# Kernel optimization log

Hardware: AMD Instinct MI355X
Metric: run time of the kernel (lower is better)

The kernel has to match this reference:

```python
import jax, jax.numpy as jnp
import numpy as np

NUM_CLASSES = 80
STRIDES = (8, 16, 32)
FEATS = ((80, 80), (40, 40), (20, 20))
RADIUS = 2.5
CAND_K = 10


def make_grids():
    grids, strides = [], []
    for (h, w), s in zip(FEATS, STRIDES):
        gx, gy = jnp.meshgrid(jnp.arange(w), jnp.arange(h))  # xy indexing: gx=col, gy=row
        g = jnp.stack([gx, gy], -1).reshape(-1, 2).astype(jnp.float32)
        grids.append(g)
        strides.append(jnp.full((h * w, 1), float(s), jnp.float32))
    return jnp.concatenate(grids, 0), jnp.concatenate(strides, 0)  # [A,2], [A,1]


def decode_level(p, s):
    # p: [B, 85, h, w] -> decoded [B, h*w, 85]; xy/wh decoded, conf/cls stay logits
    b, c, h, w = p.shape
    out = p.reshape(b, c, h * w).transpose(0, 2, 1)
    gx, gy = jnp.meshgrid(jnp.arange(w), jnp.arange(h))
    g = jnp.stack([gx, gy], -1).reshape(1, -1, 2).astype(p.dtype)
    xy = (out[..., :2] + g) * s
    wh = jnp.exp(out[..., 2:4]) * s
    return jnp.concatenate([xy, wh, out[..., 4:]], -1)


def pairwise_iou_cxcywh(a, b):
    # a: [G,4], b: [A,4] -> [G,A]
    tl = jnp.maximum(a[:, None, :2] - a[:, None, 2:] * 0.5, b[None, :, :2] - b[None, :, 2:] * 0.5)
    br = jnp.minimum(a[:, None, :2] + a[:, None, 2:] * 0.5, b[None, :, :2] + b[None, :, 2:] * 0.5)
    wh = jnp.clip(br - tl, 0.0)
    inter = wh[..., 0] * wh[..., 1]
    area_a = (a[:, 2] * a[:, 3])[:, None]
    area_b = (b[:, 2] * b[:, 3])[None, :]
    return inter / (area_a + area_b - inter + 1e-16)


def elem_iou_cxcywh(a, b):
    # a, b: [...,4] aligned -> [...]
    tl = jnp.maximum(a[..., :2] - a[..., 2:] * 0.5, b[..., :2] - b[..., 2:] * 0.5)
    br = jnp.minimum(a[..., :2] + a[..., 2:] * 0.5, b[..., :2] + b[..., 2:] * 0.5)
    wh = jnp.clip(br - tl, 0.0)
    inter = wh[..., 0] * wh[..., 1]
    area = a[..., 2] * a[..., 3] + b[..., 2] * b[..., 3]
    return inter / (area - inter + 1e-16)


def bce_logits(x, t):
    return jnp.maximum(x, 0.0) - x * t + jnp.log1p(jnp.exp(-jnp.abs(x)))


def assign_one(gt_b, gt_c, pbox, pconf, pcls, xy_center, stride_v):
    # SimOTA dynamic matching for one image. gt_b:[G,4], gt_c:[G], pbox:[A,4], pconf:[A,1], pcls:[A,C]
    G = gt_b.shape[0]
    # center-in-box / center-in-mirror(radius) masks
    bmin = gt_b[:, :2] - gt_b[:, 2:] * 0.5
    bmax = gt_b[:, :2] + gt_b[:, 2:] * 0.5
    d = jnp.concatenate([xy_center[None] - bmin[:, None], bmax[:, None] - xy_center[None]], -1)  # [G,A,4]
    in_box = jnp.min(d, -1) > 0.0
    mmin = gt_b[:, None, :2] - RADIUS * stride_v[None]
    mmax = gt_b[:, None, :2] + RADIUS * stride_v[None]
    d2 = jnp.concatenate([xy_center[None] - mmin, mmax - xy_center[None]], -1)
    in_mir = jnp.min(d2, -1) > 0.0
    union = jnp.any(in_box, 0) | jnp.any(in_mir, 0)  # [A]
    inter = in_box & in_mir  # [G,A]

    iou = pairwise_iou_cxcywh(gt_b, pbox)  # [G,A]
    iou_cost = -jnp.log(iou + 1e-8)
    # cls cost: BCE(sqrt(sigmoid(cls)*sigmoid(conf)), one_hot).sum(C), computed without [G,A,C]
    p = jnp.sqrt(jax.nn.sigmoid(pcls) * jax.nn.sigmoid(pconf))  # [A,C]
    logp = jnp.clip(jnp.log(jnp.clip(p, 1e-12)), -100.0)
    log1mp = jnp.clip(jnp.log(jnp.clip(1.0 - p, 1e-12)), -100.0)
    cls_cost = -(logp[:, gt_c].T - log1mp[:, gt_c].T + log1mp.sum(-1)[None, :])  # [G,A]

    cost = cls_cost + 3.0 * iou_cost + 1e5 * (~inter).astype(cost_dtype(pcls))
    cost = jnp.where(union[None, :], cost, 1e15)  # exclude anchors outside union (bool-index in torch)
    iou_m = jnp.where(union[None, :], iou, 0.0)

    # dynamic k per gt = clamp(int(sum top10 iou), 1)
    topk_iou, _ = jax.lax.top_k(iou_m, CAND_K)
    dyn_k = jnp.maximum(topk_iou.sum(1).astype(jnp.int32), 1)  # [G]
    _, idx = jax.lax.top_k(-cost, CAND_K)  # smallest-cost anchors per gt [G,10]
    valid = (jnp.arange(CAND_K)[None, :] < dyn_k[:, None]).astype(cost.dtype)
    mm = jnp.zeros_like(cost).at[jnp.arange(G)[:, None], idx].set(valid)  # [G,A]

    # resolve anchors matched to >1 gt by argmin cost
    multi = mm.sum(0) > 1.0
    best = jnp.argmin(cost, 0)  # [A]
    mm = jnp.where(multi[None, :], jax.nn.one_hot(best, G, dtype=mm.dtype).T, mm)

    fg = mm.sum(0) > 0.0  # [A]
    gt_idx = jnp.argmax(mm, 0)  # [A]
    match_iou = (mm * iou).sum(0)  # [A]
    return fg, gt_idx, match_iou


def cost_dtype(x):
    return x.dtype


def setup_inputs() -> dict:
    key = jax.random.key(0)
    ks = jax.random.split(key, 5)
    B, G = 32, 16
    p8 = jax.random.normal(ks[0], (B, 85, 80, 80), jnp.float32)
    p16 = jax.random.normal(ks[1], (B, 85, 40, 40), jnp.float32)
    p32 = jax.random.normal(ks[2], (B, 85, 20, 20), jnp.float32)
    u = jax.random.uniform(ks[3], (B, G, 4), jnp.float32)
    gt_boxes = jnp.concatenate([32.0 + u[..., :2] * 576.0, 16.0 + u[..., 2:] * 112.0], -1)
    gt_cls = jax.random.randint(ks[4], (B, G), 0, 80, dtype=jnp.int32)
    return {"p8": p8, "p16": p16, "p32": p32, "gt_boxes": gt_boxes, "gt_cls": gt_cls}


def reference(p8, p16, p32, gt_boxes, gt_cls):
    outs = [decode_level(p, s) for p, s in zip((p8, p16, p32), STRIDES)]
    outputs = jnp.concatenate(outs, 1)  # [B, 8400, 85]
    grids, stride_v = make_grids()
    xy_center = (grids + 0.5) * stride_v  # [A,2]
    pbox, pconf, pcls = outputs[..., :4], outputs[..., 4:5], outputs[..., 5:]

    sg = jax.lax.stop_gradient  # assignment is under torch.no_grad
    fg, gt_idx, match_iou = jax.vmap(assign_one, in_axes=(0, 0, 0, 0, 0, None, None))(
        gt_boxes, gt_cls, sg(pbox), sg(pconf), sg(pcls), xy_center, stride_v)
    match_iou = sg(match_iou)

    tgt_box = jnp.take_along_axis(gt_boxes, gt_idx[..., None], axis=1)  # [B,A,4]
    tgt_cls_id = jnp.take_along_axis(gt_cls, gt_idx, axis=1)  # [B,A]
    tgt_cls = jax.nn.one_hot(tgt_cls_id, NUM_CLASSES, dtype=outputs.dtype) * match_iou[..., None]
    fgf = fg.astype(outputs.dtype)

    iou_e = elem_iou_cxcywh(pbox, tgt_box)  # [B,A]
    loss_box = jnp.sum(fgf * (1.0 - iou_e ** 2))            # IOUloss, fg only
    loss_conf = jnp.sum(bce_logits(pconf[..., 0], fgf))     # all anchors
    loss_cls = jnp.sum(fgf[..., None] * bce_logits(pcls, tgt_cls))  # fg only
    n_fg = jnp.maximum(jnp.sum(fgf), 1.0)
    return (5.0 * loss_box + loss_conf + loss_cls) / n_fg
```

## Files before the change

kernel.cpp:

```cpp
#include <hip/hip_runtime.h>
#include <hip/hip_bf16.h>

#define A_TOT 8400
#define NB 32
#define NG 16
#define NC 80

#define K1_GX 33
#define NWAVE (K1_GX * NB * 4)
#define K3_CH 8
#define K3_W  1050

#define L2E 1.44269504088896340736f
#define LN2 0.69314718055994530942f

__device__ inline float fexp2(float x) { return __builtin_amdgcn_exp2f(x); }
__device__ inline float flog2(float x) { return __builtin_amdgcn_logf(x); }
__device__ inline float frcp(float x)  { return __builtin_amdgcn_rcpf(x); }
__device__ inline float fsqrtf_(float x) { return __builtin_amdgcn_sqrtf(x); }

__device__ inline float iou_cxcywh(float acx, float acy, float aw, float ah,
                                   float bcx, float bcy, float bw, float bh) {
    float tlx = fmaxf(acx - aw * 0.5f, bcx - bw * 0.5f);
    float tly = fmaxf(acy - ah * 0.5f, bcy - bh * 0.5f);
    float brx = fminf(acx + aw * 0.5f, bcx + bw * 0.5f);
    float bry = fminf(acy + ah * 0.5f, bcy + bh * 0.5f);
    float w = fmaxf(brx - tlx, 0.0f);
    float h = fmaxf(bry - tly, 0.0f);
    float inter = w * h;
    return inter / (aw * ah + bw * bh - inter + 1e-16f);
}

__device__ inline float dval_of(float x, float sc) {
    float u = fexp2(-x * L2E);
    float sx = frcp(1.0f + u);
    float pr = fsqrtf_(sx * sc);
    float lp  = fmaxf(LN2 * flog2(fmaxf(pr, 1e-12f)), -100.0f);
    float l1p = fmaxf(LN2 * flog2(fmaxf(1.0f - pr, 1e-12f)), -100.0f);
    return lp - l1p;
}

__device__ inline float cost_fast(float iou, float d, float sp, unsigned m, int g) {
    if (!((m >> 16) & 1u)) return 1e15f;
    float c = -(d + sp) - 3.0f * LN2 * flog2(iou + 1e-8f);
    if (!((m >> g) & 1u)) c += 100000.0f;
    return c;
}

__device__ inline unsigned long long umax64(unsigned long long a, unsigned long long b) {
    return a > b ? a : b;
}
__device__ inline unsigned long long umin64(unsigned long long a, unsigned long long b) {
    return a < b ? a : b;
}

__device__ inline const float* lvl_base(int a, int b, const float* p8, const float* p16,
                                        const float* p32, int& hw, int& HW, int& W, float& s) {
    if (a < 6400) { hw = a;        HW = 6400; W = 80; s = 8.0f;  return p8  + (size_t)b * 85 * 6400; }
    if (a < 8000) { hw = a - 6400; HW = 1600; W = 40; s = 16.0f; return p16 + (size_t)b * 85 * 1600; }
    { hw = a - 8000; HW = 400; W = 20; s = 32.0f; return p32 + (size_t)b * 85 * 400; }
}

__global__ __launch_bounds__(256) void k1_decode(
    const float* __restrict__ p8, const float* __restrict__ p16, const float* __restrict__ p32,
    const float* __restrict__ gtb,
    float4* __restrict__ pbox, float4* __restrict__ rec, float* __restrict__ part) {
    int b = blockIdx.y;
    int tid = threadIdx.x;
    int a = blockIdx.x * 256 + tid;
    float bce0_conf = 0.0f;
    if (a < A_TOT) {
        int hw, HW, W;
        float s;
        const float* base = lvl_base(a, b, p8, p16, p32, hw, HW, W, s);

        float tx = base[hw], ty = base[HW + hw];
        float tw = base[2 * HW + hw], th = base[3 * HW + hw];
        float cf = base[4 * HW + hw];
        int gx = hw % W, gy = hw / W;
        float pcx = (tx + (float)gx) * s;
        float pcy = (ty + (float)gy) * s;
        float pw = fexp2(tw * L2E) * s;
        float ph = fexp2(th * L2E) * s;

        float uc = fexp2(-cf * L2E);
        float suc = 1.0f + uc;
        float sc = frcp(suc);
        bce0_conf = cf + LN2 * flog2(suc);

        float xc = ((float)gx + 0.5f) * s;
        float yc = ((float)gy + 0.5f) * s;
        unsigned m = 0;
        bool uni = false;
        float r = 2.5f * s;
#pragma unroll 4
        for (int g = 0; g < NG; g++) {
            float gcx = gtb[(b * NG + g) * 4 + 0];
            float gcy = gtb[(b * NG + g) * 4 + 1];
            float gw  = gtb[(b * NG + g) * 4 + 2];
            float gh  = gtb[(b * NG + g) * 4 + 3];
            bool ib = (xc > gcx - gw * 0.5f) && (gcx + gw * 0.5f > xc) &&
                      (yc > gcy - gh * 0.5f) && (gcy + gh * 0.5f > yc);
            bool im = (xc > gcx - r) && (gcx + r > xc) &&
                      (yc > gcy - r) && (gcy + r > yc);
            uni |= (ib || im);
            if (ib && im) m |= (1u << g);
        }
        if (uni) m |= (1u << 16);

        float suml1p = 0.0f;
        if (uni) {
            const float* cbase = base + 5 * HW + hw;
#pragma unroll
            for (int cc = 0; cc < NC; cc += 20) {
                float x[20];
#pragma unroll
                for (int j = 0; j < 20; j++) x[j] = cbase[(cc + j) * HW];
#pragma unroll
                for (int j = 0; j < 20; j++) {
                    float u = fexp2(-x[j] * L2E);
                    float pr = fsqrtf_(frcp(1.0f + u) * sc);
                    suml1p += fmaxf(LN2 * flog2(fmaxf(1.0f - pr, 1e-12f)), -100.0f);
                }
            }
        }

        size_t i = (size_t)b * A_TOT + a;
        pbox[i] = make_float4(pcx, pcy, pw, ph);
        rec[i] = make_float4(__uint_as_float(m), sc, suml1p, cf);
    }
    float v = bce0_conf;
    for (int off = 32; off; off >>= 1) v += __shfl_down(v, off, 64);
    if ((tid & 63) == 0) {
        int wave = (blockIdx.y * gridDim.x + blockIdx.x) * 4 + (tid >> 6);
        part[wave] = v;
    }
}

__global__ __launch_bounds__(512, 4) void k2_assign(
    const float* __restrict__ gtb, const int* __restrict__ gtc,
    const float4* __restrict__ pbox, const float4* __restrict__ rec,
    const float* __restrict__ p8, const float* __restrict__ p16, const float* __restrict__ p32,
    int* __restrict__ sel, int* __restrict__ nsel) {
    __shared__ unsigned long long wred[8];
    int blk = blockIdx.x;
    int b = blk >> 4, g = blk & 15;
    int tid = threadIdx.x;

    float gcx = gtb[blk * 4 + 0], gcy = gtb[blk * 4 + 1];
    float gw = gtb[blk * 4 + 2],  gh = gtb[blk * 4 + 3];
    int cg = gtc[blk];

    unsigned long long topI[10];
    unsigned long long topC[10];
#pragma unroll
    for (int i = 0; i < 10; i++) { topI[i] = 0ull; topC[i] = 0xFFFFFFFFFFFFFFFFull; }

    for (int a = tid; a < A_TOT; a += 512) {
        size_t i = (size_t)b * A_TOT + a;
        float4 pb = pbox[i];
        float4 rc = rec[i];
        unsigned m = __float_as_uint(rc.x);
        float iou = iou_cxcywh(gcx, gcy, gw, gh, pb.x, pb.y, pb.z, pb.w);

        float cost = 1e15f;
        float mi = 0.0f;
        if ((m >> 16) & 1u) {
            mi = iou;
            int hw, HW, W;
            float s;
            const float* base = lvl_base(a, b, p8, p16, p32, hw, HW, W, s);
            float x = base[(5 + cg) * HW + hw];
            float d = dval_of(x, rc.y);
            cost = -(d + rc.z) - 3.0f * LN2 * flog2(iou + 1e-8f);
            if (!((m >> g) & 1u)) cost += 100000.0f;
        }

        if (mi > 0.0f) {
            unsigned long long kI = ((unsigned long long)__float_as_uint(mi) << 32) | (unsigned)a;
            if (kI > topI[9]) {
                unsigned long long v = kI;
#pragma unroll
                for (int i2 = 0; i2 < 10; i2++) {
                    unsigned long long big = umax64(topI[i2], v);
                    v = umin64(topI[i2], v);
                    topI[i2] = big;
                }
            }
        }
        unsigned long long kC = ((unsigned long long)__float_as_uint(cost) << 32) | (unsigned)a;
        if (kC < topC[9]) {
            unsigned long long v = kC;
#pragma unroll
            for (int i2 = 0; i2 < 10; i2++) {
                unsigned long long sml = umin64(topC[i2], v);
                v = umax64(topC[i2], v);
                topC[i2] = sml;
            }
        }
    }

    float ksum = 0.0f;
    for (int rr = 0; rr < 10; rr++) {
        unsigned long long h = topI[0];
        for (int off = 32; off; off >>= 1) h = umax64(h, __shfl_xor(h, off, 64));
        if ((tid & 63) == 0) wred[tid >> 6] = h;
        __syncthreads();
        unsigned long long w = wred[0];
#pragma unroll
        for (int j = 1; j < 8; j++) w = umax64(w, wred[j]);
        ksum += __uint_as_float((unsigned)(w >> 32));
        if (topI[0] == w) {
#pragma unroll
            for (int i = 0; i < 9; i++) topI[i] = topI[i + 1];
            topI[9] = 0ull;
        }
        __syncthreads();
    }
    int dynk = (int)ksum;
    if (dynk < 1) dynk = 1;
    if (dynk > 10) dynk = 10;

    for (int rr = 0; rr < 10; rr++) {
        unsigned long long h = topC[0];
        for (int off = 32; off; off >>= 1) h = umin64(h, __shfl_xor(h, off, 64));
        if ((tid & 63) == 0) wred[tid >> 6] = h;
        __syncthreads();
        unsigned long long w = wred[0];
#pragma unroll
        for (int j = 1; j < 8; j++) w = umin64(w, wred[j]);
        if (tid == 0) sel[blk * 10 + rr] = (int)(w & 0xffffffffu);
        if (topC[0] == w) {
#pragma unroll
            for (int i = 0; i < 9; i++) topC[i] = topC[i + 1];
            topC[9] = 0xFFFFFFFFFFFFFFFFull;
        }
        __syncthreads();
    }
    if (tid == 0) nsel[blk] = dynk;
}

__global__ __launch_bounds__(256) void k3_resolve(
    const float* __restrict__ gtb, const int* __restrict__ gtc,
    const float4* __restrict__ pbox, const float4* __restrict__ rec,
    const int* __restrict__ sel, const int* __restrict__ nsel,
    const float* __restrict__ p8, const float* __restrict__ p16, const float* __restrict__ p32,
    float4* __restrict__ part3) {
    __shared__ unsigned tag[K3_W];
    __shared__ float gb[NG * 4];
    __shared__ int gc[NG];
    __shared__ float red[256];
    int b = blockIdx.y, chunk = blockIdx.x, tid = threadIdx.x;
    int a0 = chunk * K3_W;

    for (int j = tid; j < K3_W; j += 256) tag[j] = 0;
    if (tid < NG * 4) gb[tid] = gtb[b * NG * 4 + tid];
    if (tid < NG) gc[tid] = gtc[b * NG + tid];
    __syncthreads();

    if (tid < NG * 10) {
        int g = tid / 10, k = tid % 10;
        if (k < nsel[b * NG + g]) {
            int a = sel[(b * NG + g) * 10 + k];
            if (a >= a0 && a < a0 + K3_W)
                atomicAdd(&tag[a - a0], 0x10000u + (unsigned)(g + 1));
        }
    }
    __syncthreads();

    float lbox = 0.0f, lconfc = 0.0f, lcls = 0.0f, nfg = 0.0f;
    for (int j = tid; j < K3_W; j += 256) {
        unsigned t = tag[j];
        unsigned cnt = t >> 16;
        if (!cnt) continue;
        int a = a0 + j;
        size_t i = (size_t)b * A_TOT + a;
        float4 pb = pbox[i];
        float4 rc = rec[i];
        int hw, HW, W;
        float s;
        const float* base = lvl_base(a, b, p8, p16, p32, hw, HW, W, s);
        int gs;
        if (cnt == 1) {
            gs = (int)(t & 0xffffu) - 1;
        } else {
            unsigned m = __float_as_uint(rc.x);
            float bc = 3.402823466e38f;
            gs = 0;
            for (int g = 0; g < NG; g++) {
                float iou = iou_cxcywh(gb[g * 4], gb[g * 4 + 1], gb[g * 4 + 2], gb[g * 4 + 3],
                                       pb.x, pb.y, pb.z, pb.w);
                float x = base[(5 + gc[g]) * HW + hw];
                float d = dval_of(x, rc.y);
                float c = cost_fast(iou, d, rc.z, m, g);
                if (c < bc) { bc = c; gs = g; }
            }
        }
        float miou = iou_cxcywh(gb[gs * 4], gb[gs * 4 + 1], gb[gs * 4 + 2], gb[gs * 4 + 3],
                                pb.x, pb.y, pb.z, pb.w);
        int cid = gc[gs];
        float xcid = base[(5 + cid) * HW + hw];

        float s0 = 0.0f;
        const float* cbase = base + 5 * HW + hw;
#pragma unroll
        for (int cc = 0; cc < NC; cc += 20) {
            float x[20];
#pragma unroll
            for (int jj = 0; jj < 20; jj++) x[jj] = cbase[(cc + jj) * HW];
#pragma unroll
            for (int jj = 0; jj < 20; jj++) {
                float u = fexp2(-x[jj] * L2E);
                s0 += x[jj] + LN2 * flog2(1.0f + u);
            }
        }

        lbox += 1.0f - miou * miou;
        lconfc -= rc.w;
        lcls += s0 - xcid * miou;
        nfg += 1.0f;
    }

    float vals[4] = {lbox, lconfc, lcls, nfg};
    float outv[4];
    for (int i = 0; i < 4; i++) {
        red[tid] = vals[i];
        __syncthreads();
        for (int s2 = 128; s2 > 0; s2 >>= 1) {
            if (tid < s2) red[tid] += red[tid + s2];
            __syncthreads();
        }
        outv[i] = red[0];
        __syncthreads();
    }
    if (tid == 0)
        part3[blockIdx.y * K3_CH + chunk] = make_float4(outv[0], outv[1], outv[2], outv[3]);
}

__global__ __launch_bounds__(256) void k4_final(
    const float* __restrict__ part, const float4* __restrict__ part3, float* __restrict__ out) {
    __shared__ float red[256];
    int tid = threadIdx.x;
    float v = 0.0f;
    for (int i = tid; i < NWAVE; i += 256) v += part[i];
    float4 p = part3[tid & 255];
    float vals[5] = {v, p.x, p.y, p.z, p.w};
    float tot[5];
    for (int i = 0; i < 5; i++) {
        red[tid] = vals[i];
        __syncthreads();
        for (int s2 = 128; s2 > 0; s2 >>= 1) {
            if (tid < s2) red[tid] += red[tid + s2];
            __syncthreads();
        }
        tot[i] = red[0];
        __syncthreads();
    }
    if (tid == 0) {
        float nfg = tot[4];
        if (nfg < 1.0f) nfg = 1.0f;
        out[0] = (5.0f * tot[1] + (tot[0] + tot[2]) + tot[3]) / nfg;
    }
}

extern "C" void kernel_launch(void* const* d_in, const int* in_sizes, int n_in,
                              void* d_out, int out_size, void* d_ws, size_t ws_size,
                              hipStream_t stream) {
    const float* p8  = (const float*)d_in[0];
    const float* p16 = (const float*)d_in[1];
    const float* p32 = (const float*)d_in[2];
    const float* gtb = (const float*)d_in[3];
    const int*   gtc = (const int*)d_in[4];

    char* w = (char*)d_ws;
    float4* pbox = (float4*)w;                 w += (size_t)NB * A_TOT * sizeof(float4);
    float4* rec  = (float4*)w;                 w += (size_t)NB * A_TOT * sizeof(float4);
    int* sel     = (int*)w;                    w += (size_t)NB * NG * 10 * sizeof(int);
    int* nsel    = (int*)w;                    w += (size_t)NB * NG * sizeof(int);
    float* part  = (float*)w;                  w += (size_t)NWAVE * sizeof(float);
    float4* part3 = (float4*)w;                w += (size_t)NB * K3_CH * sizeof(float4);

    k1_decode<<<dim3(K1_GX, NB), 256, 0, stream>>>(
        p8, p16, p32, gtb, pbox, rec, part);
    k2_assign<<<NB * NG, 512, 0, stream>>>(gtb, gtc, pbox, rec,
                                           p8, p16, p32, sel, nsel);
    k3_resolve<<<dim3(K3_CH, NB), 256, 0, stream>>>(gtb, gtc, pbox, rec,
                                                    sel, nsel, p8, p16, p32, part3);
    k4_final<<<1, 256, 0, stream>>>(part, part3, (float*)d_out);
}
```

Measured before the change: 185.8 us.

## Compact candidate anchors in decode, iterate only candidates in assign, fuse final reduce

The decode kernel now builds a per-image compacted list of candidate anchors (inside any GT box or radius) with shared and global atomics. It also spreads each candidate's 80-class log-sum work across four threads, so per-thread class work is balanced instead of divergent. The assign kernel iterates only that compacted list with 256 threads instead of scanning all 8400 anchors, dropping non-candidate loads and cost evaluations. The final reduction kernel is folded into the resolve kernel via a last-block-done counter, at the cost of an extra memset and atomics.

```diff
diff --git a/kernel.cpp b/kernel.cpp
--- a/kernel.cpp
+++ b/kernel.cpp
@@ -10,6 +10,7 @@
 #define NWAVE (K1_GX * NB * 4)
 #define K3_CH 8
 #define K3_W  1050
+#define K3_BLOCKS (K3_CH * NB)
 
 #define L2E 1.44269504088896340736f
 #define LN2 0.69314718055994530942f
@@ -61,15 +62,24 @@
     { hw = a - 8000; HW = 400; W = 20; s = 32.0f; return p32 + (size_t)b * 85 * 400; }
 }
 
-__global__ __launch_bounds__(256) void k1_decode(
+__global__ __launch_bounds__(256, 4) void k1_decode(
     const float* __restrict__ p8, const float* __restrict__ p16, const float* __restrict__ p32,
     const float* __restrict__ gtb,
-    float4* __restrict__ pbox, float4* __restrict__ rec, float* __restrict__ part) {
+    float4* __restrict__ pbox, float4* __restrict__ rec,
+    int* __restrict__ cmp, int* __restrict__ cnt, float* __restrict__ part) {
+    __shared__ int lcnt, base_s;
+    __shared__ int list[256];
+    __shared__ float scl[256];
     int b = blockIdx.y;
     int tid = threadIdx.x;
     int a = blockIdx.x * 256 + tid;
+    bool valid = a < A_TOT;
+    if (tid == 0) lcnt = 0;
+    __syncthreads();
+
     float bce0_conf = 0.0f;
-    if (a < A_TOT) {
+    int myslot = -1;
+    if (valid) {
         int hw, HW, W;
         float s;
         const float* base = lvl_base(a, b, p8, p16, p32, hw, HW, W, s);
@@ -106,29 +116,49 @@
             uni |= (ib || im);
             if (ib && im) m |= (1u << g);
         }
-        if (uni) m |= (1u << 16);
-
-        float suml1p = 0.0f;
         if (uni) {
-            const float* cbase = base + 5 * HW + hw;
-#pragma unroll
-            for (int cc = 0; cc < NC; cc += 20) {
-                float x[20];
-#pragma unroll
-                for (int j = 0; j < 20; j++) x[j] = cbase[(cc + j) * HW];
-#pragma unroll
-                for (int j = 0; j < 20; j++) {
-                    float u = fexp2(-x[j] * L2E);
-                    float pr = fsqrtf_(frcp(1.0f + u) * sc);
-                    suml1p += fmaxf(LN2 * flog2(fmaxf(1.0f - pr, 1e-12f)), -100.0f);
-                }
-            }
-        }
-
+            m |= (1u << 16);
+            myslot = atomicAdd(&lcnt, 1);
+            list[myslot] = tid;
+            scl[myslot] = sc;
+        }
         size_t i = (size_t)b * A_TOT + a;
         pbox[i] = make_float4(pcx, pcy, pw, ph);
-        rec[i] = make_float4(__uint_as_float(m), sc, suml1p, cf);
-    }
+        rec[i] = make_float4(__uint_as_float(m), sc, 0.0f, cf);
+    }
+    __syncthreads();
+    int n = lcnt;
+    if (tid == 0) base_s = atomicAdd(&cnt[b], n);
+    __syncthreads();
+    if (myslot >= 0) cmp[(size_t)b * A_TOT + base_s + myslot] = a;
+
+    for (int t = tid; t < n * 4; t += 256) {
+        int slot = t >> 2, q = t & 3;
+        int lt = list[slot];
+        int aa = blockIdx.x * 256 + lt;
+        float sc2 = scl[slot];
+        int hw, HW, W;
+        float s;
+        const float* base = lvl_base(aa, b, p8, p16, p32, hw, HW, W, s);
+        const float* cbase = base + (5 + q * 20) * HW + hw;
+        float x[20];
+#pragma unroll
+        for (int j = 0; j < 20; j++) x[j] = cbase[j * HW];
+        float suml1p = 0.0f;
+#pragma unroll
+        for (int j = 0; j < 20; j++) {
+            float u = fexp2(-x[j] * L2E);
+            float pr = fsqrtf_(frcp(1.0f + u) * sc2);
+            suml1p += fmaxf(LN2 * flog2(fmaxf(1.0f - pr, 1e-12f)), -100.0f);
+        }
+        suml1p += __shfl_xor(suml1p, 1, 64);
+        suml1p += __shfl_xor(suml1p, 2, 64);
+        if (q == 0) {
+            float* recf = (float*)rec;
+            recf[((size_t)b * A_TOT + aa) * 4 + 2] = suml1p;
+        }
+    }
+
     float v = bce0_conf;
     for (int off = 32; off; off >>= 1) v += __shfl_down(v, off, 64);
     if ((tid & 63) == 0) {
@@ -137,12 +167,13 @@
     }
 }
 
-__global__ __launch_bounds__(512, 4) void k2_assign(
+__global__ __launch_bounds__(256, 4) void k2_assign(
     const float* __restrict__ gtb, const int* __restrict__ gtc,
     const float4* __restrict__ pbox, const float4* __restrict__ rec,
+    const int* __restrict__ cmp, const int* __restrict__ cnt,
     const float* __restrict__ p8, const float* __restrict__ p16, const float* __restrict__ p32,
     int* __restrict__ sel, int* __restrict__ nsel) {
-    __shared__ unsigned long long wred[8];
+    __shared__ unsigned long long wred[4];
     int blk = blockIdx.x;
     int b = blk >> 4, g = blk & 15;
     int tid = threadIdx.x;
@@ -150,34 +181,31 @@
     float gcx = gtb[blk * 4 + 0], gcy = gtb[blk * 4 + 1];
     float gw = gtb[blk * 4 + 2],  gh = gtb[blk * 4 + 3];
     int cg = gtc[blk];
+    int n = cnt[b];
 
     unsigned long long topI[10];
     unsigned long long topC[10];
 #pragma unroll
     for (int i = 0; i < 10; i++) { topI[i] = 0ull; topC[i] = 0xFFFFFFFFFFFFFFFFull; }
 
-    for (int a = tid; a < A_TOT; a += 512) {
+    for (int j = tid; j < n; j += 256) {
+        int a = cmp[(size_t)b * A_TOT + j];
         size_t i = (size_t)b * A_TOT + a;
         float4 pb = pbox[i];
         float4 rc = rec[i];
         unsigned m = __float_as_uint(rc.x);
         float iou = iou_cxcywh(gcx, gcy, gw, gh, pb.x, pb.y, pb.z, pb.w);
 
-        float cost = 1e15f;
-        float mi = 0.0f;
-        if ((m >> 16) & 1u) {
-            mi = iou;
-            int hw, HW, W;
-            float s;
-            const float* base = lvl_base(a, b, p8, p16, p32, hw, HW, W, s);
-            float x = base[(5 + cg) * HW + hw];
-            float d = dval_of(x, rc.y);
-            cost = -(d + rc.z) - 3.0f * LN2 * flog2(iou + 1e-8f);
-            if (!((m >> g) & 1u)) cost += 100000.0f;
-        }
-
-        if (mi > 0.0f) {
-            unsigned long long kI = ((unsigned long long)__float_as_uint(mi) << 32) | (unsigned)a;
+        int hw, HW, W;
+        float s;
+        const float* base = lvl_base(a, b, p8, p16, p32, hw, HW, W, s);
+        float x = base[(5 + cg) * HW + hw];
+        float d = dval_of(x, rc.y);
+        float cost = -(d + rc.z) - 3.0f * LN2 * flog2(iou + 1e-8f);
+        if (!((m >> g) & 1u)) cost += 100000.0f;
+
+        if (iou > 0.0f) {
+            unsigned long long kI = ((unsigned long long)__float_as_uint(iou) << 32) | (unsigned)a;
             if (kI > topI[9]) {
                 unsigned long long v = kI;
 #pragma unroll
@@ -206,9 +234,7 @@
         for (int off = 32; off; off >>= 1) h = umax64(h, __shfl_xor(h, off, 64));
         if ((tid & 63) == 0) wred[tid >> 6] = h;
         __syncthreads();
-        unsigned long long w = wred[0];
-#pragma unroll
-        for (int j = 1; j < 8; j++) w = umax64(w, wred[j]);
+        unsigned long long w = umax64(umax64(wred[0], wred[1]), umax64(wred[2], wred[3]));
         ksum += __uint_as_float((unsigned)(w >> 32));
         if (topI[0] == w) {
 #pragma unroll
@@ -226,9 +252,7 @@
         for (int off = 32; off; off >>= 1) h = umin64(h, __shfl_xor(h, off, 64));
         if ((tid & 63) == 0) wred[tid >> 6] = h;
         __syncthreads();
-        unsigned long long w = wred[0];
-#pragma unroll
-        for (int j = 1; j < 8; j++) w = umin64(w, wred[j]);
+        unsigned long long w = umin64(umin64(wred[0], wred[1]), umin64(wred[2], wred[3]));
         if (tid == 0) sel[blk * 10 + rr] = (int)(w & 0xffffffffu);
         if (topC[0] == w) {
 #pragma unroll
@@ -245,11 +269,13 @@
     const float4* __restrict__ pbox, const float4* __restrict__ rec,
     const int* __restrict__ sel, const int* __restrict__ nsel,
     const float* __restrict__ p8, const float* __restrict__ p16, const float* __restrict__ p32,
-    float4* __restrict__ part3) {
+    const float* __restrict__ part, float4* __restrict__ part3,
+    int* __restrict__ done, float* __restrict__ out) {
     __shared__ unsigned tag[K3_W];
     __shared__ float gb[NG * 4];
     __shared__ int gc[NG];
     __shared__ float red[256];
+    __shared__ int islast;
     int b = blockIdx.y, chunk = blockIdx.x, tid = threadIdx.x;
     int a0 = chunk * K3_W;
 
@@ -271,8 +297,8 @@
     float lbox = 0.0f, lconfc = 0.0f, lcls = 0.0f, nfg = 0.0f;
     for (int j = tid; j < K3_W; j += 256) {
         unsigned t = tag[j];
-        unsigned cnt = t >> 16;
-        if (!cnt) continue;
+        unsigned cnt2 = t >> 16;
+        if (!cnt2) continue;
         int a = a0 + j;
         size_t i = (size_t)b * A_TOT + a;
         float4 pb = pbox[i];
@@ -281,7 +307,7 @@
         float s;
         const float* base = lvl_base(a, b, p8, p16, p32, hw, HW, W, s);
         int gs;
-        if (cnt == 1) {
+        if (cnt2 == 1) {
             gs = (int)(t & 0xffffu) - 1;
         } else {
             unsigned m = __float_as_uint(rc.x);
@@ -334,20 +360,21 @@
         __syncthreads();
     }
     if (tid == 0)
-        part3[blockIdx.y * K3_CH + chunk] = make_float4(outv[0], outv[1], outv[2], outv[3]);
-}
-
-__global__ __launch_bounds__(256) void k4_final(
-    const float* __restrict__ part, const float4* __restrict__ part3, float* __restrict__ out) {
-    __shared__ float red[256];
-    int tid = threadIdx.x;
+        part3[b * K3_CH + chunk] = make_float4(outv[0], outv[1], outv[2], outv[3]);
+
+    __threadfence();
+    if (tid == 0) islast = (atomicAdd(done, 1) == K3_BLOCKS - 1);
+    __syncthreads();
+    if (!islast) return;
+    __threadfence();
+
     float v = 0.0f;
     for (int i = tid; i < NWAVE; i += 256) v += part[i];
-    float4 p = part3[tid & 255];
-    float vals[5] = {v, p.x, p.y, p.z, p.w};
+    float4 p = part3[tid];
+    float fvals[5] = {v, p.x, p.y, p.z, p.w};
     float tot[5];
     for (int i = 0; i < 5; i++) {
-        red[tid] = vals[i];
+        red[tid] = fvals[i];
         __syncthreads();
         for (int s2 = 128; s2 > 0; s2 >>= 1) {
             if (tid < s2) red[tid] += red[tid + s2];
@@ -357,9 +384,9 @@
         __syncthreads();
     }
     if (tid == 0) {
-        float nfg = tot[4];
-        if (nfg < 1.0f) nfg = 1.0f;
-        out[0] = (5.0f * tot[1] + (tot[0] + tot[2]) + tot[3]) / nfg;
+        float nfg2 = tot[4];
+        if (nfg2 < 1.0f) nfg2 = 1.0f;
+        out[0] = (5.0f * tot[1] + (tot[0] + tot[2]) + tot[3]) / nfg2;
     }
 }
 
@@ -375,16 +402,21 @@
     char* w = (char*)d_ws;
     float4* pbox = (float4*)w;                 w += (size_t)NB * A_TOT * sizeof(float4);
     float4* rec  = (float4*)w;                 w += (size_t)NB * A_TOT * sizeof(float4);
+    int* cmp     = (int*)w;                    w += (size_t)NB * A_TOT * sizeof(int);
     int* sel     = (int*)w;                    w += (size_t)NB * NG * 10 * sizeof(int);
     int* nsel    = (int*)w;                    w += (size_t)NB * NG * sizeof(int);
     float* part  = (float*)w;                  w += (size_t)NWAVE * sizeof(float);
-    float4* part3 = (float4*)w;                w += (size_t)NB * K3_CH * sizeof(float4);
-
+    float4* part3 = (float4*)w;                w += (size_t)K3_BLOCKS * sizeof(float4);
+    int* ctrs    = (int*)w;                    w += (size_t)(NB + 1) * sizeof(int);
+    int* cnt = ctrs;
+    int* done = ctrs + NB;
+
+    hipMemsetAsync(ctrs, 0, (NB + 1) * sizeof(int), stream);
     k1_decode<<<dim3(K1_GX, NB), 256, 0, stream>>>(
-        p8, p16, p32, gtb, pbox, rec, part);
-    k2_assign<<<NB * NG, 512, 0, stream>>>(gtb, gtc, pbox, rec,
+        p8, p16, p32, gtb, pbox, rec, cmp, cnt, part);
+    k2_assign<<<NB * NG, 256, 0, stream>>>(gtb, gtc, pbox, rec, cmp, cnt,
                                            p8, p16, p32, sel, nsel);
     k3_resolve<<<dim3(K3_CH, NB), 256, 0, stream>>>(gtb, gtc, pbox, rec,
-                                                    sel, nsel, p8, p16, p32, part3);
-    k4_final<<<1, 256, 0, stream>>>(part, part3, (float*)d_out);
-}
+                                                    sel, nsel, p8, p16, p32,
+                                                    part, part3, done, (float*)d_out);
+}
```

Result: slower. 197.3 us (+6.2%).

## Compact candidate anchors in decode so assignment scans only candidates

Applied to the files above, without the earlier changes.

The decode kernel now appends each candidate anchor index (inside any GT box or center radius) to a per-image compacted list, using a block-local atomic counter plus one global atomic per block. The assignment kernel then loops only over that list instead of all 8400 anchors, and its block size drops from 512 to 256 threads. This is meant to cut the gather and top-k work spent on non-candidate anchors. The cost is an extra memset, atomics, a compaction buffer and an indirect load. It also changes behaviour when fewer than ten candidates exist, since non-candidate anchors are no longer considered.

```diff
diff --git a/kernel.cpp b/kernel.cpp
--- a/kernel.cpp
+++ b/kernel.cpp
@@ -10,6 +10,7 @@
 #define NWAVE (K1_GX * NB * 4)
 #define K3_CH 8
 #define K3_W  1050
+#define K3_BLOCKS (K3_CH * NB)
 
 #define L2E 1.44269504088896340736f
 #define LN2 0.69314718055994530942f
@@ -64,11 +65,17 @@
 __global__ __launch_bounds__(256) void k1_decode(
     const float* __restrict__ p8, const float* __restrict__ p16, const float* __restrict__ p32,
     const float* __restrict__ gtb,
-    float4* __restrict__ pbox, float4* __restrict__ rec, float* __restrict__ part) {
+    float4* __restrict__ pbox, float4* __restrict__ rec,
+    int* __restrict__ cmp, int* __restrict__ cnt, float* __restrict__ part) {
+    __shared__ int lcnt, base_s;
     int b = blockIdx.y;
     int tid = threadIdx.x;
     int a = blockIdx.x * 256 + tid;
+    if (tid == 0) lcnt = 0;
+    __syncthreads();
+
     float bce0_conf = 0.0f;
+    int myslot = -1;
     if (a < A_TOT) {
         int hw, HW, W;
         float s;
@@ -110,6 +117,7 @@
 
         float suml1p = 0.0f;
         if (uni) {
+            myslot = atomicAdd(&lcnt, 1);
             const float* cbase = base + 5 * HW + hw;
 #pragma unroll
             for (int cc = 0; cc < NC; cc += 20) {
@@ -129,6 +137,11 @@
         pbox[i] = make_float4(pcx, pcy, pw, ph);
         rec[i] = make_float4(__uint_as_float(m), sc, suml1p, cf);
     }
+    __syncthreads();
+    if (tid == 0) base_s = atomicAdd(&cnt[b], lcnt);
+    __syncthreads();
+    if (myslot >= 0) cmp[(size_t)b * A_TOT + base_s + myslot] = a;
+
     float v = bce0_conf;
     for (int off = 32; off; off >>= 1) v += __shfl_down(v, off, 64);
     if ((tid & 63) == 0) {
@@ -137,12 +150,13 @@
     }
 }
 
-__global__ __launch_bounds__(512, 4) void k2_assign(
+__global__ __launch_bounds__(256, 4) void k2_assign(
     const float* __restrict__ gtb, const int* __restrict__ gtc,
     const float4* __restrict__ pbox, const float4* __restrict__ rec,
+    const int* __restrict__ cmp, const int* __restrict__ cnt,
     const float* __restrict__ p8, const float* __restrict__ p16, const float* __restrict__ p32,
     int* __restrict__ sel, int* __restrict__ nsel) {
-    __shared__ unsigned long long wred[8];
+    __shared__ unsigned long long wred[4];
     int blk = blockIdx.x;
     int b = blk >> 4, g = blk & 15;
     int tid = threadIdx.x;
@@ -150,34 +164,31 @@
     float gcx = gtb[blk * 4 + 0], gcy = gtb[blk * 4 + 1];
     float gw = gtb[blk * 4 + 2],  gh = gtb[blk * 4 + 3];
     int cg = gtc[blk];
+    int n = cnt[b];
 
     unsigned long long topI[10];
     unsigned long long topC[10];
 #pragma unroll
     for (int i = 0; i < 10; i++) { topI[i] = 0ull; topC[i] = 0xFFFFFFFFFFFFFFFFull; }
 
-    for (int a = tid; a < A_TOT; a += 512) {
+    for (int j = tid; j < n; j += 256) {
+        int a = cmp[(size_t)b * A_TOT + j];
         size_t i = (size_t)b * A_TOT + a;
         float4 pb = pbox[i];
         float4 rc = rec[i];
         unsigned m = __float_as_uint(rc.x);
         float iou = iou_cxcywh(gcx, gcy, gw, gh, pb.x, pb.y, pb.z, pb.w);
 
-        float cost = 1e15f;
-        float mi = 0.0f;
-        if ((m >> 16) & 1u) {
-            mi = iou;
-            int hw, HW, W;
-            float s;
-            const float* base = lvl_base(a, b, p8, p16, p32, hw, HW, W, s);
-            float x = base[(5 + cg) * HW + hw];
-            float d = dval_of(x, rc.y);
-            cost = -(d + rc.z) - 3.0f * LN2 * flog2(iou + 1e-8f);
-            if (!((m >> g) & 1u)) cost += 100000.0f;
-        }
-
-        if (mi > 0.0f) {
-            unsigned long long kI = ((unsigned long long)__float_as_uint(mi) << 32) | (unsigned)a;
+        int hw, HW, W;
+        float s;
+        const float* base = lvl_base(a, b, p8, p16, p32, hw, HW, W, s);
+        float x = base[(5 + cg) * HW + hw];
+        float d = dval_of(x, rc.y);
+        float cost = -(d + rc.z) - 3.0f * LN2 * flog2(iou + 1e-8f);
+        if (!((m >> g) & 1u)) cost += 100000.0f;
+
+        if (iou > 0.0f) {
+            unsigned long long kI = ((unsigned long long)__float_as_uint(iou) << 32) | (unsigned)a;
             if (kI > topI[9]) {
                 unsigned long long v = kI;
 #pragma unroll
@@ -206,9 +217,7 @@
         for (int off = 32; off; off >>= 1) h = umax64(h, __shfl_xor(h, off, 64));
         if ((tid & 63) == 0) wred[tid >> 6] = h;
         __syncthreads();
-        unsigned long long w = wred[0];
-#pragma unroll
-        for (int j = 1; j < 8; j++) w = umax64(w, wred[j]);
+        unsigned long long w = umax64(umax64(wred[0], wred[1]), umax64(wred[2], wred[3]));
         ksum += __uint_as_float((unsigned)(w >> 32));
         if (topI[0] == w) {
 #pragma unroll
@@ -226,9 +235,7 @@
         for (int off = 32; off; off >>= 1) h = umin64(h, __shfl_xor(h, off, 64));
         if ((tid & 63) == 0) wred[tid >> 6] = h;
         __syncthreads();
-        unsigned long long w = wred[0];
-#pragma unroll
-        for (int j = 1; j < 8; j++) w = umin64(w, wred[j]);
+        unsigned long long w = umin64(umin64(wred[0], wred[1]), umin64(wred[2], wred[3]));
         if (tid == 0) sel[blk * 10 + rr] = (int)(w & 0xffffffffu);
         if (topC[0] == w) {
 #pragma unroll
@@ -271,8 +278,8 @@
     float lbox = 0.0f, lconfc = 0.0f, lcls = 0.0f, nfg = 0.0f;
     for (int j = tid; j < K3_W; j += 256) {
         unsigned t = tag[j];
-        unsigned cnt = t >> 16;
-        if (!cnt) continue;
+        unsigned cnt2 = t >> 16;
+        if (!cnt2) continue;
         int a = a0 + j;
         size_t i = (size_t)b * A_TOT + a;
         float4 pb = pbox[i];
@@ -281,7 +288,7 @@
         float s;
         const float* base = lvl_base(a, b, p8, p16, p32, hw, HW, W, s);
         int gs;
-        if (cnt == 1) {
+        if (cnt2 == 1) {
             gs = (int)(t & 0xffffu) - 1;
         } else {
             unsigned m = __float_as_uint(rc.x);
@@ -334,7 +341,7 @@
         __syncthreads();
     }
     if (tid == 0)
-        part3[blockIdx.y * K3_CH + chunk] = make_float4(outv[0], outv[1], outv[2], outv[3]);
+        part3[b * K3_CH + chunk] = make_float4(outv[0], outv[1], outv[2], outv[3]);
 }
 
 __global__ __launch_bounds__(256) void k4_final(
@@ -343,7 +350,7 @@
     int tid = threadIdx.x;
     float v = 0.0f;
     for (int i = tid; i < NWAVE; i += 256) v += part[i];
-    float4 p = part3[tid & 255];
+    float4 p = part3[tid];
     float vals[5] = {v, p.x, p.y, p.z, p.w};
     float tot[5];
     for (int i = 0; i < 5; i++) {
@@ -375,14 +382,17 @@
     char* w = (char*)d_ws;
     float4* pbox = (float4*)w;                 w += (size_t)NB * A_TOT * sizeof(float4);
     float4* rec  = (float4*)w;                 w += (size_t)NB * A_TOT * sizeof(float4);
+    int* cmp     = (int*)w;                    w += (size_t)NB * A_TOT * sizeof(int);
     int* sel     = (int*)w;                    w += (size_t)NB * NG * 10 * sizeof(int);
     int* nsel    = (int*)w;                    w += (size_t)NB * NG * sizeof(int);
     float* part  = (float*)w;                  w += (size_t)NWAVE * sizeof(float);
-    float4* part3 = (float4*)w;                w += (size_t)NB * K3_CH * sizeof(float4);
-
+    float4* part3 = (float4*)w;                w += (size_t)K3_BLOCKS * sizeof(float4);
+    int* cnt     = (int*)w;                    w += (size_t)NB * sizeof(int);
+
+    hipMemsetAsync(cnt, 0, NB * sizeof(int), stream);
     k1_decode<<<dim3(K1_GX, NB), 256, 0, stream>>>(
-        p8, p16, p32, gtb, pbox, rec, part);
-    k2_assign<<<NB * NG, 512, 0, stream>>>(gtb, gtc, pbox, rec,
+        p8, p16, p32, gtb, pbox, rec, cmp, cnt, part);
+    k2_assign<<<NB * NG, 256, 0, stream>>>(gtb, gtc, pbox, rec, cmp, cnt,
                                            p8, p16, p32, sel, nsel);
     k3_resolve<<<dim3(K3_CH, NB), 256, 0, stream>>>(gtb, gtc, pbox, rec,
                                                     sel, nsel, p8, p16, p32, part3);
```

Result: faster. 174.7 us (-6.0%).
